# Optimization experiments

Hardware: AMD Instinct MI355X
Metric: run time of the kernel (lower is better)

## Reference

```python
import jax, jax.numpy as jnp
import numpy as np

NUM_HEADS = 4
WS = 3


def setup_inputs() -> dict:
    key = jax.random.key(0)
    k1, k2, k3 = jax.random.split(key, 3)
    B, Hs, Ws_, C = 16, 96, 96, 256
    x = jax.random.normal(k1, (B, Hs * Ws_, C), dtype=jnp.float32)
    # torch nn.Linear weights: [out_features, in_features]
    Wqkv = jax.random.normal(k2, (3 * C, C), dtype=jnp.float32) * (1.0 / np.sqrt(C))
    Wproj = jax.random.normal(k3, (C, C), dtype=jnp.float32) * (1.0 / np.sqrt(C))
    return {"x": x, "Wqkv": Wqkv, "Wproj": Wproj, "H": Hs, "W": Ws_}


def reference(x, Wqkv, Wproj, H, W):
    B, N, C = x.shape
    ws = WS
    nh = NUM_HEADS
    hd = C // nh
    scale = hd ** -0.5

    pad_h = (ws - H % ws) % ws
    pad_w = (ws - W % ws) % ws
    xg = x.reshape(B, H, W, C)
    if pad_h > 0 or pad_w > 0:
        xg = jnp.pad(xg, ((0, 0), (0, pad_h), (0, pad_w), (0, 0)))
    H_pad, W_pad = H + pad_h, W + pad_w
    nWh, nWw = H_pad // ws, W_pad // ws
    Bw = B * nWh * nWw

    # window partition: [B, nWh, ws, nWw, ws, C] -> [Bw, ws*ws, C]
    xw = xg.reshape(B, nWh, ws, nWw, ws, C).transpose(0, 1, 3, 2, 4, 5)
    xw = xw.reshape(Bw, ws * ws, C)

    # qkv projection (Linear, no bias): x @ W^T
    qkv = xw @ Wqkv.T                                   # [Bw, 9, 3C]
    qkv = qkv.reshape(Bw, ws * ws, 3, nh, hd).transpose(2, 0, 3, 1, 4)
    q, k, v = qkv[0], qkv[1], qkv[2]                    # [Bw, nh, 9, hd]

    attn = jnp.einsum("bhqd,bhkd->bhqk", q, k) * scale  # [Bw, nh, 9, 9]
    attn = jax.nn.softmax(attn, axis=-1)
    out = jnp.einsum("bhqk,bhkd->bhqd", attn, v)        # [Bw, nh, 9, hd]
    out = out.transpose(0, 2, 1, 3).reshape(Bw, ws * ws, C)
    out = out @ Wproj.T

    # window unpartition
    out = out.reshape(B, nWh, nWw, ws, ws, C).transpose(0, 1, 3, 2, 4, 5)
    out = out.reshape(B, H_pad, W_pad, C)
    if pad_h > 0 or pad_w > 0:
        out = out[:, :H, :W, :]
    return out.reshape(B, H * W, C)
```

## Files before the change

kernel.cpp:

```cpp
#include <hip/hip_runtime.h>
#include <hip/hip_bf16.h>

using f32x4  = __attribute__((ext_vector_type(4))) float;
using bf16x8 = __attribute__((ext_vector_type(8))) short;
using bf16x4 = __attribute__((ext_vector_type(4))) short;
using u32x2  = __attribute__((ext_vector_type(2))) unsigned int;
using u32x4  = __attribute__((ext_vector_type(4))) unsigned int;

__device__ __forceinline__ float bf2f(short s) {
    unsigned u = ((unsigned)(unsigned short)s) << 16;
    return __builtin_bit_cast(float, u);
}
__device__ __forceinline__ unsigned short f2b(float f) {
    unsigned u = __builtin_bit_cast(unsigned, f);
    unsigned r = u + 0x7FFFu + ((u >> 16) & 1u);
    return (unsigned short)(r >> 16);
}
__device__ __forceinline__ void gl_lds16(const void* g, void* l) {
    __builtin_amdgcn_global_load_lds((const __attribute__((address_space(1))) void*)g,
                                     (__attribute__((address_space(3))) void*)l, 16, 0, 0);
}

__global__ void k_wconv(const float* __restrict__ wq, const float* __restrict__ wp,
                        unsigned short* __restrict__ out) {
    int i = blockIdx.x * 256 + threadIdx.x;
    float v = (i < 196608) ? wq[i] : wp[i - 196608];
    out[i] = f2b(v);
}

__global__ __launch_bounds__(256) void k_cvt(const float* __restrict__ x,
                                             unsigned short* __restrict__ xb) {
    const int NG = 4718592;
    for (int g = blockIdx.x * 256 + threadIdx.x; g < NG; g += 524288) {
        const f32x4* p = (const f32x4*)(x + (size_t)g * 8);
        f32x4 a = p[0], b = p[1];
        bf16x8 v;
#pragma unroll
        for (int j = 0; j < 4; ++j) {
            v[j]     = (short)f2b(a[j]);
            v[4 + j] = (short)f2b(b[j]);
        }
        *(bf16x8*)(xb + (size_t)g * 8) = v;
    }
}

__global__ __launch_bounds__(256) void k_qkv(
    const unsigned short* __restrict__ xb,
    const unsigned short* __restrict__ wqkv,
    unsigned short* __restrict__ qkv)
{
    __shared__ unsigned short As[128 * 64];
    __shared__ unsigned short Bs[128 * 64];
    const int tid = threadIdx.x;
    const int wv = tid >> 6, ln = tid & 63;
    const int lr = ln & 15, lk = ln >> 4;
    const int l8 = ln >> 3, c8 = ln & 7;

    int b = blockIdx.x;
    int w = (b & 7) * 864 + (b >> 3);
    const int n0 = (w / 1152) * 128;
    const int m0 = (w % 1152) * 128;
    const int mq = (wv >> 1) * 64, nq = (wv & 1) * 64;

    f32x4 acc[4][4];
#pragma unroll
    for (int mi = 0; mi < 4; ++mi)
#pragma unroll
        for (int ni = 0; ni < 4; ++ni) {
            f32x4 z = {0.f, 0.f, 0.f, 0.f};
            acc[mi][ni] = z;
        }

#pragma unroll 1
    for (int ks = 0; ks < 4; ++ks) {
        const int k0 = ks * 64;
        __syncthreads();
#pragma unroll
        for (int i = 0; i < 4; ++i) {
            int r8 = i * 8 + l8;
            int sc = (c8 ^ (r8 & 7)) * 8;
            gl_lds16(xb   + (size_t)(m0 + wv * 32 + r8) * 256 + k0 + sc,
                     &As[(wv * 32 + i * 8) * 64]);
            gl_lds16(wqkv + (size_t)(n0 + wv * 32 + r8) * 256 + k0 + sc,
                     &Bs[(wv * 32 + i * 8) * 64]);
        }
        __syncthreads();

#pragma unroll
        for (int kk = 0; kk < 2; ++kk) {
            bf16x8 av[4], bv[4];
#pragma unroll
            for (int i = 0; i < 4; ++i) {
                int ar = mq + i * 16 + lr;
                av[i] = *(const bf16x8*)&As[ar * 64 + (((kk * 4 + lk) ^ (ar & 7)) * 8)];
                int br = nq + i * 16 + lr;
                bv[i] = *(const bf16x8*)&Bs[br * 64 + (((kk * 4 + lk) ^ (br & 7)) * 8)];
            }
#pragma unroll
            for (int mi = 0; mi < 4; ++mi)
#pragma unroll
                for (int ni = 0; ni < 4; ++ni)
                    acc[mi][ni] = __builtin_amdgcn_mfma_f32_16x16x32_bf16(bv[ni], av[mi], acc[mi][ni], 0, 0, 0);
        }
    }

#pragma unroll
    for (int mi = 0; mi < 4; ++mi) {
        const size_t row = m0 + mq + mi * 16 + lr;
#pragma unroll
        for (int ni = 0; ni < 4; ++ni) {
            u32x2 u;
            u[0] = (unsigned)f2b(acc[mi][ni][0]) | ((unsigned)f2b(acc[mi][ni][1]) << 16);
            u[1] = (unsigned)f2b(acc[mi][ni][2]) | ((unsigned)f2b(acc[mi][ni][3]) << 16);
            *(u32x2*)(qkv + row * 768 + n0 + nq + ni * 16 + lk * 4) = u;
        }
    }
}

__global__ __launch_bounds__(256) void k_attn(
    unsigned short* __restrict__ qkv)
{
    constexpr int LQ = 68;
    __shared__ unsigned short Ks[144 * LQ];
    __shared__ unsigned short Vs[144 * LQ];
    const int tid = threadIdx.x;
    const int t3 = blockIdx.x;
    const int hf = blockIdx.y;
    const int h  = blockIdx.z;
    const int bb = t3 >> 5, wh = t3 & 31;

    for (int idx = tid; idx < 1152; idx += 256) {
        int row = idx >> 3, ch = idx & 7;
        int ww = row / 9, t = row - ww * 9;
        int rr = t / 3, cc = t - rr * 3;
        size_t xrow = (size_t)bb * 9216 + (wh * 3 + rr) * 96 + hf * 48 + ww * 3 + cc;
        *(bf16x8*)&Ks[row * LQ + ch * 8] = *(const bf16x8*)(qkv + xrow * 768 + 256 + h * 64 + ch * 8);
        *(bf16x8*)&Vs[row * LQ + ch * 8] = *(const bf16x8*)(qkv + xrow * 768 + 512 + h * 64 + ch * 8);
    }
    __syncthreads();

#pragma unroll 1
    for (int pass = 0; pass < 2; ++pass) {
        int row;
        bool act;
        if (pass == 0) { row = tid >> 1;            act = true; }
        else           { row = 128 + (tid >> 1);    act = tid < 32; }
        if (act) {
            const int hc = tid & 1;
            const int w9 = (row / 9) * 9;
            int t = row - w9;
            int rr = t / 3, cc = t - rr * 3;
            size_t xrow = (size_t)bb * 9216 + (wh * 3 + rr) * 96 + hf * 48 + (w9 / 9) * 3 + cc;
            unsigned short* qp = qkv + xrow * 768 + h * 64 + hc * 32;
            float q[32];
#pragma unroll
            for (int g = 0; g < 4; ++g) {
                bf16x8 v = *(const bf16x8*)(qp + g * 8);
#pragma unroll
                for (int j = 0; j < 8; ++j) q[g * 8 + j] = bf2f(v[j]);
            }
            float s[9];
#pragma unroll
            for (int kk = 0; kk < 9; ++kk) {
                float acc = 0.f;
#pragma unroll
                for (int g = 0; g < 4; ++g) {
                    bf16x8 v = *(const bf16x8*)&Ks[(w9 + kk) * LQ + hc * 32 + g * 8];
#pragma unroll
                    for (int j = 0; j < 8; ++j) acc += q[g * 8 + j] * bf2f(v[j]);
                }
                s[kk] = acc;
            }
#pragma unroll
            for (int kk = 0; kk < 9; ++kk)
                s[kk] = (s[kk] + __shfl_xor(s[kk], 1)) * 0.125f;
            float m = s[0];
#pragma unroll
            for (int kk = 1; kk < 9; ++kk) m = fmaxf(m, s[kk]);
            float sum = 0.f;
#pragma unroll
            for (int kk = 0; kk < 9; ++kk) { s[kk] = __expf(s[kk] - m); sum += s[kk]; }
            float inv = 1.f / sum;
            float o[32];
#pragma unroll
            for (int d = 0; d < 32; ++d) o[d] = 0.f;
#pragma unroll
            for (int kk = 0; kk < 9; ++kk) {
                float pk = s[kk] * inv;
#pragma unroll
                for (int g = 0; g < 4; ++g) {
                    bf16x8 v = *(const bf16x8*)&Vs[(w9 + kk) * LQ + hc * 32 + g * 8];
#pragma unroll
                    for (int j = 0; j < 8; ++j) o[g * 8 + j] += pk * bf2f(v[j]);
                }
            }
#pragma unroll
            for (int grp = 0; grp < 4; ++grp) {
                u32x4 u;
#pragma unroll
                for (int e = 0; e < 4; ++e) {
                    int i0 = grp * 8 + e * 2;
                    u[e] = (unsigned)f2b(o[i0]) | ((unsigned)f2b(o[i0 + 1]) << 16);
                }
                *(u32x4*)(qp + grp * 8) = u;
            }
        }
    }
}

__global__ __launch_bounds__(256) void k_proj(
    const unsigned short* __restrict__ ain,
    const unsigned short* __restrict__ wproj,
    float* __restrict__ out)
{
    __shared__ unsigned short As[128 * 64];
    __shared__ unsigned short Bs[128 * 64];
    const int tid = threadIdx.x;
    const int wv = tid >> 6, ln = tid & 63;
    const int lr = ln & 15, lk = ln >> 4;
    const int l8 = ln >> 3, c8 = ln & 7;

    int b = blockIdx.x;
    int w = (b & 7) * 288 + (b >> 3);
    const int n0 = (w / 1152) * 128;
    const int m0 = (w % 1152) * 128;
    const int mq = (wv >> 1) * 64, nq = (wv & 1) * 64;

    f32x4 acc[4][4];
#pragma unroll
    for (int mi = 0; mi < 4; ++mi)
#pragma unroll
        for (int ni = 0; ni < 4; ++ni) {
            f32x4 z = {0.f, 0.f, 0.f, 0.f};
            acc[mi][ni] = z;
        }

#pragma unroll 1
    for (int ks = 0; ks < 4; ++ks) {
        const int k0 = ks * 64;
        __syncthreads();
#pragma unroll
        for (int i = 0; i < 4; ++i) {
            int r8 = i * 8 + l8;
            int sc = (c8 ^ (r8 & 7)) * 8;
            gl_lds16(ain   + (size_t)(m0 + wv * 32 + r8) * 768 + k0 + sc,
                     &As[(wv * 32 + i * 8) * 64]);
            gl_lds16(wproj + (size_t)(n0 + wv * 32 + r8) * 256 + k0 + sc,
                     &Bs[(wv * 32 + i * 8) * 64]);
        }
        __syncthreads();

#pragma unroll
        for (int kk = 0; kk < 2; ++kk) {
            bf16x8 av[4], bv[4];
#pragma unroll
            for (int i = 0; i < 4; ++i) {
                int ar = mq + i * 16 + lr;
                av[i] = *(const bf16x8*)&As[ar * 64 + (((kk * 4 + lk) ^ (ar & 7)) * 8)];
                int br = nq + i * 16 + lr;
                bv[i] = *(const bf16x8*)&Bs[br * 64 + (((kk * 4 + lk) ^ (br & 7)) * 8)];
            }
#pragma unroll
            for (int mi = 0; mi < 4; ++mi)
#pragma unroll
                for (int ni = 0; ni < 4; ++ni)
                    acc[mi][ni] = __builtin_amdgcn_mfma_f32_16x16x32_bf16(bv[ni], av[mi], acc[mi][ni], 0, 0, 0);
        }
    }

#pragma unroll
    for (int mi = 0; mi < 4; ++mi) {
        const size_t row = m0 + mq + mi * 16 + lr;
#pragma unroll
        for (int ni = 0; ni < 4; ++ni)
            *(f32x4*)&out[row * 256 + n0 + nq + ni * 16 + lk * 4] = acc[mi][ni];
    }
}


__device__ __forceinline__ int grow_of(int wbase, int row) {
    int wi = row / 9;
    int t  = row - wi * 9;
    int w  = wbase + wi;
    if (w >= 16384) return -1;
    int b = w >> 10, rem = w & 1023;
    int wh = rem >> 5, ww = rem & 31;
    int r = t / 3, c = t - r * 3;
    return b * 9216 + (wh * 3 + r) * 96 + ww * 3 + c;
}

__global__ __launch_bounds__(256) void k_winattn_fb(
    const float* __restrict__ x,
    const unsigned short* __restrict__ wqkv,
    unsigned short* __restrict__ aout)
{
    constexpr int LDA = 264;
    constexpr int LQ  = 68;
    __shared__ unsigned short As[64 * LDA];
    __shared__ unsigned short Qb[3][64 * LQ];
    __shared__ int rowmap[64];

    const int tid = threadIdx.x;
    const int wbase = blockIdx.x * 7;
    const int wv = tid >> 6, ln = tid & 63;
    const int lr = ln & 15, lk = ln >> 4;
    const int mw = wv >> 1, nw = wv & 1;

    if (tid < 64)
        rowmap[tid] = (tid < 63) ? grow_of(wbase, tid) : -1;
    __syncthreads();

    for (int idx = tid; idx < 64 * 32; idx += 256) {
        int row = idx >> 5, g = idx & 31;
        int gr = rowmap[row];
        bf16x8 v;
        if (gr >= 0) {
            const f32x4* p = (const f32x4*)(x + (size_t)gr * 256 + g * 8);
            f32x4 f0 = p[0], f1 = p[1];
#pragma unroll
            for (int j = 0; j < 4; ++j) {
                v[j]     = (short)f2b(f0[j]);
                v[4 + j] = (short)f2b(f1[j]);
            }
        } else {
#pragma unroll
            for (int j = 0; j < 8; ++j) v[j] = 0;
        }
        *(bf16x8*)&As[row * LDA + g * 8] = v;
    }
    __syncthreads();

#pragma unroll 1
    for (int h = 0; h < 4; ++h) {
#pragma unroll 1
        for (int part = 0; part < 3; ++part) {
            const int j0 = part * 256 + h * 64 + nw * 32;
            bf16x8 w[2][8];
#pragma unroll
            for (int ni = 0; ni < 2; ++ni)
#pragma unroll
                for (int kk = 0; kk < 8; ++kk)
                    w[ni][kk] = *(const bf16x8*)(wqkv + (size_t)(j0 + ni * 16 + lr) * 256 + kk * 32 + lk * 8);

            f32x4 acc[2][2];
#pragma unroll
            for (int mi = 0; mi < 2; ++mi)
#pragma unroll
                for (int ni = 0; ni < 2; ++ni) {
                    f32x4 z = {0.f, 0.f, 0.f, 0.f};
                    acc[mi][ni] = z;
                }
#pragma unroll
            for (int kk = 0; kk < 8; ++kk) {
                const int k0 = kk * 32 + lk * 8;
                bf16x8 a0 = *(const bf16x8*)&As[(mw * 32 + lr) * LDA + k0];
                bf16x8 a1 = *(const bf16x8*)&As[(mw * 32 + 16 + lr) * LDA + k0];
                acc[0][0] = __builtin_amdgcn_mfma_f32_16x16x32_bf16(w[0][kk], a0, acc[0][0], 0, 0, 0);
                acc[1][0] = __builtin_amdgcn_mfma_f32_16x16x32_bf16(w[0][kk], a1, acc[1][0], 0, 0, 0);
                acc[0][1] = __builtin_amdgcn_mfma_f32_16x16x32_bf16(w[1][kk], a0, acc[0][1], 0, 0, 0);
                acc[1][1] = __builtin_amdgcn_mfma_f32_16x16x32_bf16(w[1][kk], a1, acc[1][1], 0, 0, 0);
            }
#pragma unroll
            for (int mi = 0; mi < 2; ++mi)
#pragma unroll
                for (int ni = 0; ni < 2; ++ni) {
                    int row = mw * 32 + mi * 16 + lr;
                    int col = nw * 32 + ni * 16 + lk * 4;
                    u32x2 u;
                    u[0] = (unsigned)f2b(acc[mi][ni][0]) | ((unsigned)f2b(acc[mi][ni][1]) << 16);
                    u[1] = (unsigned)f2b(acc[mi][ni][2]) | ((unsigned)f2b(acc[mi][ni][3]) << 16);
                    *(u32x2*)&Qb[part][row * LQ + col] = u;
                }
        }
        __syncthreads();
        {
            const int row = wv * 16 + lr;
            const int c   = lk;
            if (row < 63) {
                const int w9 = (row / 9) * 9;
                float q[16];
#pragma unroll
                for (int g = 0; g < 4; ++g) {
                    bf16x4 v = *(const bf16x4*)&Qb[0][row * LQ + c * 16 + g * 4];
#pragma unroll
                    for (int j = 0; j < 4; ++j) q[g * 4 + j] = bf2f(v[j]);
                }
                float s[9];
#pragma unroll
                for (int kk = 0; kk < 9; ++kk) {
                    float t = 0.f;
#pragma unroll
                    for (int g = 0; g < 4; ++g) {
                        bf16x4 v = *(const bf16x4*)&Qb[1][(w9 + kk) * LQ + c * 16 + g * 4];
#pragma unroll
                        for (int j = 0; j < 4; ++j) t += q[g * 4 + j] * bf2f(v[j]);
                    }
                    s[kk] = t;
                }
#pragma unroll
                for (int kk = 0; kk < 9; ++kk) {
                    float t = s[kk];
                    t += __shfl_xor(t, 16);
                    t += __shfl_xor(t, 32);
                    s[kk] = t * 0.125f;
                }
                float m = s[0];
#pragma unroll
                for (int kk = 1; kk < 9; ++kk) m = fmaxf(m, s[kk]);
                float sum = 0.f;
#pragma unroll
                for (int kk = 0; kk < 9; ++kk) { s[kk] = __expf(s[kk] - m); sum += s[kk]; }
                float inv = 1.f / sum;
                float o[16];
#pragma unroll
                for (int d = 0; d < 16; ++d) o[d] = 0.f;
#pragma unroll
                for (int kk = 0; kk < 9; ++kk) {
                    float pk = s[kk] * inv;
#pragma unroll
                    for (int g = 0; g < 4; ++g) {
                        bf16x4 v = *(const bf16x4*)&Qb[2][(w9 + kk) * LQ + c * 16 + g * 4];
#pragma unroll
                        for (int j = 0; j < 4; ++j) o[g * 4 + j] += pk * bf2f(v[j]);
                    }
                }
                const int gr = rowmap[row];
                if (gr >= 0) {
#pragma unroll
                    for (int half = 0; half < 2; ++half) {
                        u32x4 u;
#pragma unroll
                        for (int e = 0; e < 4; ++e) {
                            int i0 = half * 8 + e * 2;
                            u[e] = (unsigned)f2b(o[i0]) | ((unsigned)f2b(o[i0 + 1]) << 16);
                        }
                        *(u32x4*)(aout + (size_t)gr * 256 + h * 64 + c * 16 + half * 8) = u;
                    }
                }
            }
        }
        __syncthreads();
    }
}

__global__ __launch_bounds__(256) void k_proj_fb(
    const unsigned short* __restrict__ ain,
    const unsigned short* __restrict__ wproj,
    float* __restrict__ out)
{
    const int tid = threadIdx.x;
    const int wv = tid >> 6, ln = tid & 63;
    const int lr = ln & 15, lk = ln >> 4;
    const size_t row0 = (size_t)blockIdx.x * 128;

    bf16x8 af[2][8];
#pragma unroll
    for (int mi = 0; mi < 2; ++mi) {
        const size_t row = row0 + wv * 32 + mi * 16 + lr;
#pragma unroll
        for (int kk = 0; kk < 8; ++kk)
            af[mi][kk] = *(const bf16x8*)(ain + row * 256 + kk * 32 + lk * 8);
    }
#pragma unroll
    for (int nc = 0; nc < 4; ++nc) {
        const int j0 = nc * 64;
        f32x4 acc[2][4];
#pragma unroll
        for (int mi = 0; mi < 2; ++mi)
#pragma unroll
            for (int ni = 0; ni < 4; ++ni) {
                f32x4 z = {0.f, 0.f, 0.f, 0.f};
                acc[mi][ni] = z;
            }
#pragma unroll
        for (int kk = 0; kk < 8; ++kk) {
            bf16x8 w[4];
#pragma unroll
            for (int ni = 0; ni < 4; ++ni)
                w[ni] = *(const bf16x8*)(wproj + (size_t)(j0 + ni * 16 + lr) * 256 + kk * 32 + lk * 8);
#pragma unroll
            for (int ni = 0; ni < 4; ++ni) {
                acc[0][ni] = __builtin_amdgcn_mfma_f32_16x16x32_bf16(w[ni], af[0][kk], acc[0][ni], 0, 0, 0);
                acc[1][ni] = __builtin_amdgcn_mfma_f32_16x16x32_bf16(w[ni], af[1][kk], acc[1][ni], 0, 0, 0);
            }
        }
#pragma unroll
        for (int mi = 0; mi < 2; ++mi) {
            const size_t row = row0 + wv * 32 + mi * 16 + lr;
#pragma unroll
            for (int ni = 0; ni < 4; ++ni)
                *(f32x4*)&out[row * 256 + j0 + ni * 16 + lk * 4] = acc[mi][ni];
        }
    }
}

extern "C" void kernel_launch(void* const* d_in, const int* in_sizes, int n_in,
                              void* d_out, int out_size, void* d_ws, size_t ws_size,
                              hipStream_t stream) {
    const float* x  = (const float*)d_in[0];
    const float* wq = (const float*)d_in[1];
    const float* wp = (const float*)d_in[2];
    unsigned short* wsb     = (unsigned short*)d_ws;
    unsigned short* wqkv_b  = wsb;
    unsigned short* wproj_b = wsb + 196608;
    float* out = (float*)d_out;

    k_wconv<<<1024, 256, 0, stream>>>(wq, wp, wsb);

    const size_t need = (262144ULL + 37748736ULL + 113246208ULL) * 2ULL;
    if (ws_size >= need) {
        unsigned short* xb  = wsb + 262144;
        unsigned short* qkv = xb + 37748736;
        k_cvt <<<2048, 256, 0, stream>>>(x, xb);
        k_qkv <<<6912, 256, 0, stream>>>(xb, wqkv_b, qkv);
        k_attn<<<dim3(512, 2, 4), 256, 0, stream>>>(qkv);
        k_proj<<<2304, 256, 0, stream>>>(qkv, wproj_b, out);
    } else {
        unsigned short* aout = wsb + 262144;
        k_winattn_fb<<<2341, 256, 0, stream>>>(x, wqkv_b, aout);
        k_proj_fb  <<<1152, 256, 0, stream>>>(aout, wproj_b, out);
    }
}
```

Before: 309.0 us.

## Fuse fp32-to-bf16 input conversion into QKV GEMM with full-K A tile reuse

Result: faster. 300.3 us (-2.8%).

```diff
diff --git a/kernel.cpp b/kernel.cpp
--- a/kernel.cpp
+++ b/kernel.cpp
@@ -28,91 +28,92 @@
     out[i] = f2b(v);
 }
 
-__global__ __launch_bounds__(256) void k_cvt(const float* __restrict__ x,
-                                             unsigned short* __restrict__ xb) {
-    const int NG = 4718592;
-    for (int g = blockIdx.x * 256 + threadIdx.x; g < NG; g += 524288) {
-        const f32x4* p = (const f32x4*)(x + (size_t)g * 8);
-        f32x4 a = p[0], b = p[1];
-        bf16x8 v;
-#pragma unroll
-        for (int j = 0; j < 4; ++j) {
-            v[j]     = (short)f2b(a[j]);
-            v[4 + j] = (short)f2b(b[j]);
-        }
-        *(bf16x8*)(xb + (size_t)g * 8) = v;
-    }
-}
-
-__global__ __launch_bounds__(256) void k_qkv(
-    const unsigned short* __restrict__ xb,
+__global__ __launch_bounds__(256) void k_qkv2(
+    const float* __restrict__ x,
     const unsigned short* __restrict__ wqkv,
     unsigned short* __restrict__ qkv)
 {
-    __shared__ unsigned short As[128 * 64];
+    __shared__ unsigned short As[128 * 256];
     __shared__ unsigned short Bs[128 * 64];
     const int tid = threadIdx.x;
     const int wv = tid >> 6, ln = tid & 63;
     const int lr = ln & 15, lk = ln >> 4;
     const int l8 = ln >> 3, c8 = ln & 7;
 
-    int b = blockIdx.x;
-    int w = (b & 7) * 864 + (b >> 3);
-    const int n0 = (w / 1152) * 128;
-    const int m0 = (w % 1152) * 128;
+    const int b = blockIdx.x;
+    const int w = (b & 7) * 144 + (b >> 3);
+    const size_t m0 = (size_t)w * 128;
     const int mq = (wv >> 1) * 64, nq = (wv & 1) * 64;
 
-    f32x4 acc[4][4];
-#pragma unroll
-    for (int mi = 0; mi < 4; ++mi)
-#pragma unroll
-        for (int ni = 0; ni < 4; ++ni) {
-            f32x4 z = {0.f, 0.f, 0.f, 0.f};
-            acc[mi][ni] = z;
-        }
+#pragma unroll
+    for (int i = 0; i < 16; ++i) {
+        int idx = tid + 256 * i;
+        int row = idx >> 5, ch = idx & 31;
+        const f32x4* p = (const f32x4*)(x + (m0 + row) * 256 + ch * 8);
+        f32x4 f0 = p[0], f1 = p[1];
+        bf16x8 v;
+#pragma unroll
+        for (int j = 0; j < 4; ++j) {
+            v[j]     = (short)f2b(f0[j]);
+            v[4 + j] = (short)f2b(f1[j]);
+        }
+        *(bf16x8*)&As[row * 256 + (ch ^ (row & 7)) * 8] = v;
+    }
+    __syncthreads();
 
 #pragma unroll 1
-    for (int ks = 0; ks < 4; ++ks) {
-        const int k0 = ks * 64;
-        __syncthreads();
-#pragma unroll
-        for (int i = 0; i < 4; ++i) {
-            int r8 = i * 8 + l8;
-            int sc = (c8 ^ (r8 & 7)) * 8;
-            gl_lds16(xb   + (size_t)(m0 + wv * 32 + r8) * 256 + k0 + sc,
-                     &As[(wv * 32 + i * 8) * 64]);
-            gl_lds16(wqkv + (size_t)(n0 + wv * 32 + r8) * 256 + k0 + sc,
-                     &Bs[(wv * 32 + i * 8) * 64]);
-        }
-        __syncthreads();
-
-#pragma unroll
-        for (int kk = 0; kk < 2; ++kk) {
-            bf16x8 av[4], bv[4];
+    for (int nc = 0; nc < 6; ++nc) {
+        const int n0 = nc * 128;
+        f32x4 acc[4][4];
+#pragma unroll
+        for (int mi = 0; mi < 4; ++mi)
+#pragma unroll
+            for (int ni = 0; ni < 4; ++ni) {
+                f32x4 z = {0.f, 0.f, 0.f, 0.f};
+                acc[mi][ni] = z;
+            }
+
+#pragma unroll 1
+        for (int ks = 0; ks < 4; ++ks) {
+            __syncthreads();
 #pragma unroll
             for (int i = 0; i < 4; ++i) {
-                int ar = mq + i * 16 + lr;
-                av[i] = *(const bf16x8*)&As[ar * 64 + (((kk * 4 + lk) ^ (ar & 7)) * 8)];
-                int br = nq + i * 16 + lr;
-                bv[i] = *(const bf16x8*)&Bs[br * 64 + (((kk * 4 + lk) ^ (br & 7)) * 8)];
-            }
-#pragma unroll
-            for (int mi = 0; mi < 4; ++mi)
-#pragma unroll
-                for (int ni = 0; ni < 4; ++ni)
-                    acc[mi][ni] = __builtin_amdgcn_mfma_f32_16x16x32_bf16(bv[ni], av[mi], acc[mi][ni], 0, 0, 0);
-        }
-    }
-
-#pragma unroll
-    for (int mi = 0; mi < 4; ++mi) {
-        const size_t row = m0 + mq + mi * 16 + lr;
-#pragma unroll
-        for (int ni = 0; ni < 4; ++ni) {
-            u32x2 u;
-            u[0] = (unsigned)f2b(acc[mi][ni][0]) | ((unsigned)f2b(acc[mi][ni][1]) << 16);
-            u[1] = (unsigned)f2b(acc[mi][ni][2]) | ((unsigned)f2b(acc[mi][ni][3]) << 16);
-            *(u32x2*)(qkv + row * 768 + n0 + nq + ni * 16 + lk * 4) = u;
+                int r8 = i * 8 + l8;
+                int sc = (c8 ^ (r8 & 7)) * 8;
+                gl_lds16(wqkv + (size_t)(n0 + wv * 32 + r8) * 256 + ks * 64 + sc,
+                         &Bs[(wv * 32 + i * 8) * 64]);
+            }
+            __syncthreads();
+
+#pragma unroll
+            for (int kk = 0; kk < 2; ++kk) {
+                bf16x8 av[4], bv[4];
+#pragma unroll
+                for (int i = 0; i < 4; ++i) {
+                    int ar = mq + i * 16 + lr;
+                    int ch = ks * 8 + kk * 4 + lk;
+                    av[i] = *(const bf16x8*)&As[ar * 256 + ((ch ^ (ar & 7)) * 8)];
+                    int br = nq + i * 16 + lr;
+                    bv[i] = *(const bf16x8*)&Bs[br * 64 + (((kk * 4 + lk) ^ (br & 7)) * 8)];
+                }
+#pragma unroll
+                for (int mi = 0; mi < 4; ++mi)
+#pragma unroll
+                    for (int ni = 0; ni < 4; ++ni)
+                        acc[mi][ni] = __builtin_amdgcn_mfma_f32_16x16x32_bf16(bv[ni], av[mi], acc[mi][ni], 0, 0, 0);
+            }
+        }
+
+#pragma unroll
+        for (int mi = 0; mi < 4; ++mi) {
+            const size_t row = m0 + mq + mi * 16 + lr;
+#pragma unroll
+            for (int ni = 0; ni < 4; ++ni) {
+                u32x2 u;
+                u[0] = (unsigned)f2b(acc[mi][ni][0]) | ((unsigned)f2b(acc[mi][ni][1]) << 16);
+                u[1] = (unsigned)f2b(acc[mi][ni][2]) | ((unsigned)f2b(acc[mi][ni][3]) << 16);
+                *(u32x2*)(qkv + row * 768 + n0 + nq + ni * 16 + lk * 4) = u;
+            }
         }
     }
 }
@@ -507,12 +508,10 @@
 
     k_wconv<<<1024, 256, 0, stream>>>(wq, wp, wsb);
 
-    const size_t need = (262144ULL + 37748736ULL + 113246208ULL) * 2ULL;
+    const size_t need = 524288ULL + 147456ULL * 768ULL * 2ULL;
     if (ws_size >= need) {
-        unsigned short* xb  = wsb + 262144;
-        unsigned short* qkv = xb + 37748736;
-        k_cvt <<<2048, 256, 0, stream>>>(x, xb);
-        k_qkv <<<6912, 256, 0, stream>>>(xb, wqkv_b, qkv);
+        unsigned short* qkv = wsb + 262144;
+        k_qkv2<<<1152, 256, 0, stream>>>(x, wqkv_b, qkv);
         k_attn<<<dim3(512, 2, 4), 256, 0, stream>>>(qkv);
         k_proj<<<2304, 256, 0, stream>>>(qkv, wproj_b, out);
     } else {
```
